# Performance work log

Measured on AMD Instinct MI355X. Metric: run time of the kernel, lower is better.

## Reference

```python
import jax, jax.numpy as jnp
import numpy as np

N = 50000      # nodes
E = 800000     # edges (avg degree 16)
D_IN = 128     # input_dim
H = 64         # hidden_dim (== output_dim)
L = 3          # num_layers


def setup_inputs() -> dict:
    key = jax.random.key(0)
    ks = jax.random.split(key, 24)
    s = 0.05
    p = lambda k, shape: jax.random.normal(k, shape, dtype=jnp.float32) * s
    inp = {}
    inp["node_features"] = jax.random.normal(ks[0], (N, D_IN), dtype=jnp.float32)
    inp["edge_index"] = jax.random.randint(ks[1], (2, E), 0, N, dtype=jnp.int32)
    # pre_mlp: Linear-ReLU-Linear (setup_LRL_nn with hidden_sizes=[hidden_dim])
    inp["pre_w1"] = p(ks[2], (D_IN, H)); inp["pre_b1"] = jnp.zeros((H,), jnp.float32)
    inp["pre_w2"] = p(ks[3], (H, H));    inp["pre_b2"] = jnp.zeros((H,), jnp.float32)
    # learnable skip gates (initialized to ones as in the module)
    inp["skip"] = jnp.ones((L, L), jnp.float32)
    # SAGEConv layers: lin_l (on mean-aggregated neighbors, with bias) + lin_r (root)
    for i in range(L):
        din = H * (i + 1)
        inp[f"wl{i}"] = p(ks[4 + 3 * i], (din, H))
        inp[f"bl{i}"] = jnp.zeros((H,), jnp.float32)
        inp[f"wr{i}"] = p(ks[5 + 3 * i], (din, H))
    # post_mlp: 256->64, 64->64, 64->256, 256->64
    inp["post_w1"] = p(ks[14], (H * (L + 1), H)); inp["post_b1"] = jnp.zeros((H,), jnp.float32)
    inp["post_w2"] = p(ks[15], (H, H));           inp["post_b2"] = jnp.zeros((H,), jnp.float32)
    inp["post_w3"] = p(ks[16], (H, 256));         inp["post_b3"] = jnp.zeros((256,), jnp.float32)
    inp["post_w4"] = p(ks[17], (256, H));         inp["post_b4"] = jnp.zeros((H,), jnp.float32)
    return inp


def _sage(x, src, dst, inv_deg, wl, bl, wr):
    # PyG SAGEConv (mean aggr): lin_l(mean_{j->i} x_j) + lin_r(x_i)
    agg = jax.ops.segment_sum(x[src], dst, num_segments=N) * inv_deg  # [N, Din]
    return agg @ wl + bl + x @ wr


def reference(node_features, edge_index,
              pre_w1, pre_b1, pre_w2, pre_b2, skip,
              wl0, bl0, wr0, wl1, bl1, wr1, wl2, bl2, wr2,
              post_w1, post_b1, post_w2, post_b2, post_w3, post_b3, post_w4, post_b4):
    src, dst = edge_index[0], edge_index[1]
    deg = jax.ops.segment_sum(jnp.ones((E,), jnp.float32), dst, num_segments=N)
    inv_deg = (1.0 / jnp.maximum(deg, 1.0))[:, None]  # [N,1]

    # pre_mlp
    x = jax.nn.relu(node_features @ pre_w1 + pre_b1) @ pre_w2 + pre_b2  # [N,H]

    layers = [(wl0, bl0, wr0), (wl1, bl1, wr1), (wl2, bl2, wr2)]
    all_emb = [x]
    emb = x
    for i, (wl, bl, wr) in enumerate(layers):
        gates = jax.nn.sigmoid(skip[i, :i + 1])  # [i+1]
        curr = jnp.concatenate([all_emb[j] * gates[j] for j in range(i + 1)], axis=1)  # [N, H*(i+1)]
        h = jax.nn.relu(_sage(curr, src, dst, inv_deg, wl, bl, wr))  # [N,H]  (dropout p=0)
        emb = jnp.concatenate([emb, h], axis=1)
        all_emb.append(h)

    s = jnp.sum(emb, axis=-2)  # sums over all nodes -> [H*(L+1)] (faithful to source)
    h = jax.nn.leaky_relu(s @ post_w1 + post_b1, negative_slope=0.1)
    h = jax.nn.relu(h @ post_w2 + post_b2)
    h = jax.nn.relu(h @ post_w3 + post_b3)
    return h @ post_w4 + post_b4  # [H]
```

## Files before the change

### kernel.cpp

```cpp
#include <hip/hip_runtime.h>
#include <math.h>

#define NN 50000
#define NE 800000
#define NB 196
#define PBH 8192

typedef float v4f __attribute__((ext_vector_type(4)));
typedef float v2f __attribute__((ext_vector_type(2)));
typedef _Float16 v8h __attribute__((ext_vector_type(8)));

__device__ __forceinline__ unsigned char enc8(float v) {
#if __has_builtin(__builtin_amdgcn_cvt_pk_fp8_f32)
  return (unsigned char)(__builtin_amdgcn_cvt_pk_fp8_f32(v, v, 0, false) & 0xFF);
#else
  unsigned u = __float_as_uint(v);
  unsigned s = (u >> 24) & 0x80u;
  unsigned au = u & 0x7fffffffu;
  float a = __uint_as_float(au);
  if (au < 0x3C800000u) {
    int m = (int)(a * 512.0f + 0.5f);
    if (m >= 8) return (unsigned char)(s | 8u);
    return (unsigned char)(s | (unsigned)m);
  }
// ... 18 lines not shown
}
#endif

__device__ __forceinline__ void dec8x8(uint2 u, float* f) {
#ifdef DEC8_HW
  v2f p0 = __builtin_amdgcn_cvt_pk_f32_fp8((int)u.x, false);
  v2f p1 = __builtin_amdgcn_cvt_pk_f32_fp8((int)u.x, true);
  v2f p2 = __builtin_amdgcn_cvt_pk_f32_fp8((int)u.y, false);
  v2f p3 = __builtin_amdgcn_cvt_pk_f32_fp8((int)u.y, true);
  f[0] = p0.x; f[1] = p0.y; f[2] = p1.x; f[3] = p1.y;
  f[4] = p2.x; f[5] = p2.y; f[6] = p3.x; f[7] = p3.y;
#else
#pragma unroll
  for (int i = 0; i < 4; ++i) f[i] = dec8_1((u.x >> (8 * i)) & 0xFF);
#pragma unroll
  for (int i = 0; i < 4; ++i) f[4 + i] = dec8_1((u.y >> (8 * i)) & 0xFF);
#endif
}
__device__ __forceinline__ void dec8x16(uint4 u, float* f) {
  dec8x8(make_uint2(u.x, u.y), f);
  dec8x8(make_uint2(u.z, u.w), f + 8);
}


__global__ __launch_bounds__(256) void k_bhist(const int* __restrict__ dst,
                                               int* __restrict__ gbcnt) {
  __shared__ int lcnt[NB];
  int t = threadIdx.x;
  for (int i = t; i < NB; i += 256) lcnt[i] = 0;
  __syncthreads();
  int eb = blockIdx.x * 4096;
#pragma unroll
  for (int i = 0; i < 16; ++i) {
    int e = eb + i * 256 + t;
    if (e < NE) atomicAdd(&lcnt[dst[e] >> 8], 1);
  }
  __syncthreads();
  for (int i = t; i < NB; i += 256)
    if (lcnt[i]) atomicAdd(&gbcnt[i], lcnt[i]);
}

__global__ __launch_bounds__(256) void k_bscan(const int* __restrict__ gbcnt,
                                               int* __restrict__ boff,
                                               int* __restrict__ gcur,
                                               int* __restrict__ offs,
                                               float* __restrict__ sv) {
// ... 102 lines not shown
#pragma unroll
  for (int i = 0; i < 4; ++i)
    *(float4*)&sw[i * 1024 + t * 4] = *(const float4*)(w + i * 1024 + t * 4);
  float gs = 1.f;
  if (A.gidx[b] >= 0) gs = 1.f / (1.f + __expf(-A.skip[A.gidx[b]]));
  __syncthreads();
#pragma unroll
  for (int i = 0; i < 4; ++i) {
    int u = t * 4 + i;
    int lane = u & 63, ct = (u >> 6) & 3, hl = (u >> 8) & 1, ks = (u >> 9) & 1;
    v8h val;
#pragma unroll
    for (int j = 0; j < 8; ++j) {
      int k = ks * 32 + ((lane >> 4) & 3) * 8 + j;
      int n = ct * 16 + (lane & 15);
      float f = sw[k * 64 + n] * gs;
      _Float16 h = (_Float16)f;
      val[j] = hl ? (_Float16)(f - (float)h) : h;
    }
    *(v8h*)(A.outp + (size_t)b * PBH + (size_t)u * 8) = val;
  }
}

struct LinArgs {
  const _Float16* a[6];
  int pb[6];
  int nsrc;
  int fusedsrc;
  const unsigned char* feat8;
  const int* offs;
  const int* csr;
  const float* invd;
  _Float16* mout;
  const _Float16* wp;
  const float* bias;
  _Float16* outp;
  unsigned char* out8;
  float* colsum;
  int n;
  int relu;
};

__global__ __launch_bounds__(512) void k_linear(LinArgs A) {
  __shared__ _Float16 atile[64 * 72];
  __shared__ float cbuf[64 * 65];
  const int t    = threadIdx.x;
  const int lane = t & 63;
  const int w    = t >> 6;
  const int wq   = w & 3;
  const int sg   = w >> 2;
  const int qd   = lane >> 4;
  const int ln   = lane & 15;
  const int n0   = blockIdx.x * 64;

  if (A.fusedsrc >= 0) {
    const int nd = t >> 3;
    const int sl = (t >> 2) & 1;
    const int q  = t & 3;
    const int node = n0 + nd;
    float a[16];
#pragma unroll
    for (int i = 0; i < 16; ++i) a[i] = 0.f;
    float dinv = 0.f;
    if (node < A.n) {
      int s = A.offs[node], e = A.offs[node + 1];
      dinv = A.invd[node];
      const unsigned char* fb = A.feat8;
      if (e > s) {
        int emax = e - 1;
        for (int p0 = s; p0 < e; p0 += 8) {
          int pa = p0 + sl, pb_ = p0 + 2 + sl, pc = p0 + 4 + sl, pd = p0 + 6 + sl;
          int ja = __builtin_nontemporal_load(A.csr + (pa < emax ? pa : emax));
          int jb = __builtin_nontemporal_load(A.csr + (pb_ < emax ? pb_ : emax));
          int jc = __builtin_nontemporal_load(A.csr + (pc < emax ? pc : emax));
          int jd = __builtin_nontemporal_load(A.csr + (pd < emax ? pd : emax));
          uint4 ua = *(const uint4*)(fb + (size_t)ja * 64 + q * 16);
          uint4 ub = *(const uint4*)(fb + (size_t)jb * 64 + q * 16);
          uint4 uc = *(const uint4*)(fb + (size_t)jc * 64 + q * 16);
          uint4 ud = *(const uint4*)(fb + (size_t)jd * 64 + q * 16);
          float f[16];
          dec8x16(ua, f);
          if (pa < e) {
#pragma unroll
            for (int i = 0; i < 16; ++i) a[i] += f[i];
          }
          dec8x16(ub, f);
          if (pb_ < e) {
#pragma unroll
            for (int i = 0; i < 16; ++i) a[i] += f[i];
          }
          dec8x16(uc, f);
          if (pc < e) {
#pragma unroll
            for (int i = 0; i < 16; ++i) a[i] += f[i];
          }
          dec8x16(ud, f);
          if (pd < e) {
#pragma unroll
            for (int i = 0; i < 16; ++i) a[i] += f[i];
          }
        }
      }
    }
#pragma unroll
    for (int i = 0; i < 16; ++i) a[i] += __shfl_xor(a[i], 4, 64);
    if (sl == 0) {
      v8h o0, o1;
#pragma unroll
      for (int i = 0; i < 8; ++i) {
        o0[i] = (_Float16)(a[i] * dinv);
        o1[i] = (_Float16)(a[8 + i] * dinv);
      }
      *(v8h*)(&atile[nd * 72 + q * 16]) = o0;
      *(v8h*)(&atile[nd * 72 + q * 16 + 8]) = o1;
      if (A.mout && node < A.n) {
        *(v8h*)(A.mout + (size_t)node * 64 + q * 16) = o0;
        *(v8h*)(A.mout + (size_t)node * 64 + q * 16 + 8) = o1;
      }
    }
  }
  __syncthreads();

  v4f acc[4];
#pragma unroll
  for (int ct = 0; ct < 4; ++ct) acc[ct] = (v4f){0.f, 0.f, 0.f, 0.f};

  const int arow = n0 + wq * 16 + ln;
  const bool arv = arow < A.n;
  const int h = (A.nsrc + 1) >> 1;
  const int sbeg = sg ? h : 0;
  const int send = sg ? A.nsrc : h;
  v8h ah[2];

  for (int s = sbeg; s < send; ++s) {
    if (s == A.fusedsrc) {
      const _Float16* ph = atile + (wq * 16 + ln) * 72;
      ah[0] = *(const v8h*)(ph + qd * 8);
      ah[1] = *(const v8h*)(ph + 32 + qd * 8);
    } else if (arv) {
      const _Float16* ph = A.a[s] + (size_t)arow * 64;
      ah[0] = *(const v8h*)(ph + qd * 8);
      ah[1] = *(const v8h*)(ph + 32 + qd * 8);
    } else {
      v8h z;
#pragma unroll
      for (int j = 0; j < 8; ++j) z[j] = (_Float16)0.f;
      ah[0] = ah[1] = z;
    }
    const _Float16* pw = A.wp + (size_t)A.pb[s] * PBH;
#pragma unroll
    for (int ks = 0; ks < 2; ++ks) {
#pragma unroll
      for (int ct = 0; ct < 4; ++ct) {
        const _Float16* pf = pw + (size_t)(ks * 512 + ct * 64 + lane) * 8;
        v8h bh = *(const v8h*)(pf);
        v8h bl = *(const v8h*)(pf + 256 * 8);
        acc[ct] = __builtin_amdgcn_mfma_f32_16x16x32_f16(ah[ks], bh, acc[ct], 0, 0, 0);
        acc[ct] = __builtin_amdgcn_mfma_f32_16x16x32_f16(ah[ks], bl, acc[ct], 0, 0, 0);
      }
    }
  }

  if (sg == 1) {
#pragma unroll
    for (int ct = 0; ct < 4; ++ct)
#pragma unroll
      for (int r = 0; r < 4; ++r) {
        int nb = wq * 16 + qd * 4 + r;
        cbuf[nb * 65 + ct * 16 + ln] = acc[ct][r];
      }
  }
  __syncthreads();

  unsigned char* f8t = (unsigned char*)atile;
  float* red = (float*)&atile[2304];

  if (sg == 0) {
    float bvals[4];
#pragma unroll
    for (int ct = 0; ct < 4; ++ct) bvals[ct] = A.bias[ct * 16 + ln];
    float cs[4] = {0.f, 0.f, 0.f, 0.f};
#pragma unroll
    for (int ct = 0; ct < 4; ++ct) {
#pragma unroll
      for (int r = 0; r < 4; ++r) {
        int nb = wq * 16 + qd * 4 + r;
        int node = n0 + nb;
        float v = acc[ct][r] + cbuf[nb * 65 + ct * 16 + ln] + bvals[ct];
        if (A.relu) v = fmaxf(v, 0.f);
        if (node < A.n) {
          if (A.outp) A.outp[(size_t)node * 64 + ct * 16 + ln] = (_Float16)v;
          if (A.out8) f8t[nb * 64 + ct * 16 + ln] = enc8(v);
          cs[ct] += v;
        }
      }
    }
    if (A.colsum) {
#pragma unroll
      for (int ct = 0; ct < 4; ++ct) {
        float v = cs[ct];
        v += __shfl_xor(v, 16, 64);
        v += __shfl_xor(v, 32, 64);
        if (qd == 0) red[wq * 64 + ct * 16 + ln] = v;
      }
    }
  }
  if (A.out8 || A.colsum) __syncthreads();
  if (A.out8 && t < 256) {
    int row = t >> 2, ch = t & 3;
    if (n0 + row < A.n) {
      uint4 val = *(const uint4*)(f8t + row * 64 + ch * 16);
      *(uint4*)(A.out8 + (size_t)(n0 + row) * 64 + ch * 16) = val;
    }
  }
  if (A.colsum && t < 64) {
    float ssum = red[t] + red[64 + t] + red[128 + t] + red[192 + t];
    atomicAdd(&A.colsum[t], ssum);
  }
}

__global__ __launch_bounds__(256) void k_pre(
    const float* __restrict__ nf, const _Float16* __restrict__ wp,
    const float* __restrict__ b1, const float* __restrict__ b2,
    _Float16* __restrict__ xout, unsigned char* __restrict__ x8,
    float* __restrict__ colsum, int n) {
  __shared__ _Float16 atile[64 * 72];
  const int t    = threadIdx.x;
  const int lane = t & 63;
  const int wv   = t >> 6;
  const int qd   = lane >> 4;
  const int ln   = lane & 15;
  const int n0   = blockIdx.x * 64;
  const int arow = n0 + wv * 16 + ln;
  const bool arv = arow < n;

  v4f acc[4];
#pragma unroll
  for (int ct = 0; ct < 4; ++ct) acc[ct] = (v4f){0.f, 0.f, 0.f, 0.f};
  v8h ah[2];

  auto domfma = [&](int pbi) {
    const _Float16* pw = wp + (size_t)pbi * PBH;
#pragma unroll
    for (int ks = 0; ks < 2; ++ks) {
#pragma unroll
      for (int ct = 0; ct < 4; ++ct) {
        const _Float16* pf = pw + (size_t)(ks * 512 + ct * 64 + lane) * 8;
        v8h bh = *(const v8h*)(pf);
        v8h bl = *(const v8h*)(pf + 256 * 8);
        acc[ct] = __builtin_amdgcn_mfma_f32_16x16x32_f16(ah[ks], bh, acc[ct], 0, 0, 0);
        acc[ct] = __builtin_amdgcn_mfma_f32_16x16x32_f16(ah[ks], bl, acc[ct], 0, 0, 0);
      }
    }
  };

  for (int s = 0; s < 2; ++s) {
#pragma unroll
    for (int ks = 0; ks < 2; ++ks) {
      v8h hv;
      if (arv) {
        const float* p = nf + (size_t)arow * 128 + s * 64 + ks * 32 + qd * 8;
        float4 u0 = *(const float4*)(p);
        float4 u1 = *(const float4*)(p + 4);
        hv[0] = (_Float16)u0.x; hv[1] = (_Float16)u0.y;
        hv[2] = (_Float16)u0.z; hv[3] = (_Float16)u0.w;
        hv[4] = (_Float16)u1.x; hv[5] = (_Float16)u1.y;
        hv[6] = (_Float16)u1.z; hv[7] = (_Float16)u1.w;
      } else {
#pragma unroll
        for (int j = 0; j < 8; ++j) hv[j] = (_Float16)0.f;
      }
      ah[ks] = hv;
    }
    domfma(s);
  }

  float b1v[4];
#pragma unroll
  for (int ct = 0; ct < 4; ++ct) b1v[ct] = b1[ct * 16 + ln];
#pragma unroll
  for (int ct = 0; ct < 4; ++ct) {
#pragma unroll
    for (int r = 0; r < 4; ++r) {
      int nb = wv * 16 + qd * 4 + r;
      float v = fmaxf(acc[ct][r] + b1v[ct], 0.f);
      atile[nb * 72 + ct * 16 + ln] = (_Float16)v;
    }
  }
#pragma unroll
  for (int ct = 0; ct < 4; ++ct) acc[ct] = (v4f){0.f, 0.f, 0.f, 0.f};
  __syncthreads();

  {
    const _Float16* ph = atile + (wv * 16 + ln) * 72;
    ah[0] = *(const v8h*)(ph + qd * 8);
    ah[1] = *(const v8h*)(ph + 32 + qd * 8);
  }
  domfma(2);

  float b2v[4];
#pragma unroll
  for (int ct = 0; ct < 4; ++ct) b2v[ct] = b2[ct * 16 + ln];

  __syncthreads();
  unsigned char* f8t = (unsigned char*)atile;
  float* red = (float*)&atile[2304];
  float cs[4] = {0.f, 0.f, 0.f, 0.f};
#pragma unroll
  for (int ct = 0; ct < 4; ++ct) {
#pragma unroll
    for (int r = 0; r < 4; ++r) {
      int nb = wv * 16 + qd * 4 + r;
      int node = n0 + nb;
      float v = acc[ct][r] + b2v[ct];
      if (node < n) {
        xout[(size_t)node * 64 + ct * 16 + ln] = (_Float16)v;
        f8t[nb * 64 + ct * 16 + ln] = enc8(v);
        cs[ct] += v;
      }
    }
  }
#pragma unroll
  for (int ct = 0; ct < 4; ++ct) {
    float v = cs[ct];
    v += __shfl_xor(v, 16, 64);
    v += __shfl_xor(v, 32, 64);
    if (qd == 0) red[wv * 64 + ct * 16 + ln] = v;
  }
  __syncthreads();
  {
    int row = t >> 2, ch = t & 3;
    if (n0 + row < n) {
      uint4 val = *(const uint4*)(f8t + row * 64 + ch * 16);
      *(uint4*)(x8 + (size_t)(n0 + row) * 64 + ch * 16) = val;
    }
  }
  if (t < 64) {
    float ssum = red[t] + red[64 + t] + red[128 + t] + red[192 + t];
    atomicAdd(&colsum[t], ssum);
  }
}

__global__ __launch_bounds__(256) void k_post(const float* __restrict__ s,
                                              const float* __restrict__ w1, const float* __restrict__ b1,
                                              const float* __restrict__ w2, const float* __restrict__ b2,
                                              const float* __restrict__ w3, const float* __restrict__ b3,
                                              const float* __restrict__ w4, const float* __restrict__ b4,
                                              float* __restrict__ outp) {
  __shared__ float sh[256], h1[64], h2[64], h3[256];
  int t = threadIdx.x;
  sh[t] = s[t];
  __syncthreads();
  if (t < 64) {
    float a = b1[t];
    for (int k = 0; k < 256; ++k) a += sh[k] * w1[k * 64 + t];
    h1[t] = (a >= 0.f) ? a : 0.1f * a;
  }
  __syncthreads();
  if (t < 64) {
    float a = b2[t];
    for (int k = 0; k < 64; ++k) a += h1[k] * w2[k * 64 + t];
    h2[t] = fmaxf(a, 0.f);
  }
  __syncthreads();
  {
    float a = b3[t];
    for (int k = 0; k < 64; ++k) a += h2[k] * w3[k * 256 + t];
    h3[t] = fmaxf(a, 0.f);
  }
  __syncthreads();
  if (t < 64) {
    float a = b4[t];
    for (int k = 0; k < 256; ++k) a += h3[k] * w4[k * 64 + t];
    outp[t] = a;
  }
}

extern "C" void kernel_launch(void* const* d_in, const int* in_sizes, int n_in,
                              void* d_out, int out_size, void* d_ws, size_t ws_size,
                              hipStream_t stream) {
  const float* nf     = (const float*)d_in[0];
  const int*   ei     = (const int*)d_in[1];
  const float* pre_w1 = (const float*)d_in[2];
  const float* pre_b1 = (const float*)d_in[3];
  const float* pre_w2 = (const float*)d_in[4];
  const float* pre_b2 = (const float*)d_in[5];
  const float* skip   = (const float*)d_in[6];
  const float* wl0 = (const float*)d_in[7],  *bl0 = (const float*)d_in[8],  *wr0 = (const float*)d_in[9];
  const float* wl1 = (const float*)d_in[10], *bl1 = (const float*)d_in[11], *wr1 = (const float*)d_in[12];
  const float* wl2 = (const float*)d_in[13], *bl2 = (const float*)d_in[14], *wr2 = (const float*)d_in[15];
  const float* pw1 = (const float*)d_in[16], *pb1 = (const float*)d_in[17];
  const float* pw2 = (const float*)d_in[18], *pb2 = (const float*)d_in[19];
  const float* pw3 = (const float*)d_in[20], *pb3 = (const float*)d_in[21];
  const float* pw4 = (const float*)d_in[22], *pb4 = (const float*)d_in[23];
  float* out = (float*)d_out;

  const int N = NN, E = NE;

  char* ws = (char*)d_ws;
  size_t pos = 0;
  auto alloc = [&](size_t bytes) {
    char* p = ws + pos;
    pos += (bytes + 255) & ~(size_t)255;
    return (void*)p;
  };
  int*      gbcnt = (int*)alloc((size_t)NB * 4);
  int*      boff  = (int*)alloc((size_t)(NB + 1) * 4);
  int*      gcur  = (int*)alloc((size_t)NB * 4);
  unsigned* ebuf  = (unsigned*)alloc((size_t)E * 4);
  int*      offs  = (int*)alloc((size_t)(N + 1) * 4);
  float*    invd  = (float*)alloc((size_t)N * 4);
  int*      csr   = (int*)alloc((size_t)E * 4);
  const size_t PB = (size_t)N * 64 * 2;
  _Float16* x  = (_Float16*)alloc(PB);
  _Float16* h0 = (_Float16*)alloc(PB);
  _Float16* h1 = (_Float16*)alloc(PB);
  _Float16* m0 = (_Float16*)alloc(PB);
  _Float16* m1 = (_Float16*)alloc(PB);
  unsigned char* f8 = (unsigned char*)alloc((size_t)N * 64);
  _Float16* wpk = (_Float16*)alloc((size_t)15 * PBH * 2);
  float* sv = (float*)alloc(256 * 4);

  hipMemsetAsync(gbcnt, 0, (size_t)NB * 4, stream);

  {
    WPackArgs W;
    const float* wsrc[15] = {pre_w1, pre_w1 + 64 * 64, pre_w2,
                             wl0, wr0,
                             wl1, wl1 + 64 * 64, wr1, wr1 + 64 * 64,
                             wl2, wl2 + 64 * 64, wl2 + 128 * 64,
                             wr2, wr2 + 64 * 64, wr2 + 128 * 64};
    const int gi[15] = {-1, -1, -1, 0, 0, 3, 4, 3, 4, 6, 7, 8, 6, 7, 8};
    for (int i = 0; i < 15; ++i) { W.w[i] = wsrc[i]; W.gidx[i] = gi[i]; }
    W.skip = skip; W.outp = wpk;
    k_wpack<<<15, 256, 0, stream>>>(W);
  }

  const int* e_src = ei;
  const int* e_dst = ei + E;
  const int EGRID = (E + 4095) / 4096;
  k_bhist<<<EGRID, 256, 0, stream>>>(e_dst, gbcnt);
  k_bscan<<<1, 256, 0, stream>>>(gbcnt, boff, gcur, offs, sv);
  k_bscatter<<<EGRID, 256, 0, stream>>>(e_src, e_dst, gcur, ebuf);
  k_bbuild<<<NB, 256, 0, stream>>>(ebuf, boff, offs, invd, csr);

  const int LGRID = (N + 63) / 64;
  auto lin = [&](int nsrc, int fusedsrc, _Float16* mout,
                 const _Float16* a0, int p0, const _Float16* a1, int p1,
                 const _Float16* a2, int p2, const _Float16* a3, int p3,
                 const _Float16* a4, int p4, const _Float16* a5, int p5,
                 const float* bias, _Float16* op, unsigned char* o8,
                 float* colsum, int relu) {
    LinArgs A;
    A.a[0] = a0; A.a[1] = a1; A.a[2] = a2; A.a[3] = a3; A.a[4] = a4; A.a[5] = a5;
    A.pb[0] = p0; A.pb[1] = p1; A.pb[2] = p2; A.pb[3] = p3; A.pb[4] = p4; A.pb[5] = p5;
    A.nsrc = nsrc; A.fusedsrc = fusedsrc;
    A.feat8 = f8; A.offs = offs; A.csr = csr; A.invd = invd;
    A.mout = mout; A.wp = wpk;
    A.bias = bias; A.outp = op; A.out8 = o8; A.colsum = colsum;
    A.n = N; A.relu = relu;
    k_linear<<<LGRID, 512, 0, stream>>>(A);
  };

  k_pre<<<LGRID, 256, 0, stream>>>(nf, wpk, pre_b1, pre_b2, x, f8, sv, N);

  lin(2, 0, m0,
      nullptr, 3, x, 4,
      nullptr, 0, nullptr, 0, nullptr, 0, nullptr, 0,
      bl0, h0, f8, sv + 64, 1);

  lin(4, 1, m1,
      m0, 5, nullptr, 6, x, 7, h0, 8,
      nullptr, 0, nullptr, 0,
      bl1, h1, f8, sv + 128, 1);

  lin(6, 2, nullptr,
      m0, 9, m1, 10, nullptr, 11, x, 12, h0, 13, h1, 14,
      bl2, nullptr, nullptr, sv + 192, 1);

  k_post<<<1, 256, 0, stream>>>(sv, pw1, pb1, pw2, pb2, pw3, pb3, pw4, pb4, out);
}
```

Before: 334.5 us.

## Fuse graph build and all layers into two cooperative grid-synced kernels

```diff
diff --git a/kernel.cpp b/kernel.cpp
--- a/kernel.cpp
+++ b/kernel.cpp
@@ -1,5 +1,8 @@
 #include <hip/hip_runtime.h>
+#include <hip/hip_cooperative_groups.h>
 #include <math.h>
+
+namespace cg = cooperative_groups;
 
 #define NN 50000
 #define NE 800000
@@ -64,6 +67,484 @@
   dec8x8(make_uint2(u.z, u.w), f + 8);
 }
 
+struct GArgs {
+  const int* esrc; const int* edst;
+  int* gbcnt; int* boff; int* gcur; int* offs; float* invd; int* csr;
+  unsigned* ebuf; float* sv;
+  const float* w[15]; int gidx[15]; const float* skip; _Float16* wpk;
+};
+
+__global__ __launch_bounds__(256) void k_graph(GArgs A) {
+  cg::grid_group grid = cg::this_grid();
+  __shared__ int s0[NB];
+  __shared__ int s1[256];
+  __shared__ int s2[256];
+  __shared__ float sw[4096];
+  const int b = blockIdx.x, t = threadIdx.x;
+
+  if (t == 0) A.gbcnt[b] = 0;
+  if (b == 0) A.sv[t] = 0.f;
+  grid.sync();
+
+  for (int i = t; i < NB; i += 256) s0[i] = 0;
+  __syncthreads();
+  const int eb = b * 4096;
+#pragma unroll
+  for (int i = 0; i < 16; ++i) {
+    int e = eb + i * 256 + t;
+    if (e < NE) atomicAdd(&s0[A.edst[e] >> 8], 1);
+  }
+  __syncthreads();
+  for (int i = t; i < NB; i += 256)
+    if (s0[i]) atomicAdd(&A.gbcnt[i], s0[i]);
+  grid.sync();
+
+  if (b == 0) {
+    int v = (t < NB) ? A.gbcnt[t] : 0;
+    s1[t] = v;
+    __syncthreads();
+    for (int o = 1; o < 256; o <<= 1) {
+      int u = (t >= o) ? s1[t - o] : 0;
+      __syncthreads();
+      s1[t] += u;
+      __syncthreads();
+    }
+    if (t < NB) { int x = s1[t] - v; A.boff[t] = x; A.gcur[t] = x; }
+    if (t == NB - 1) A.boff[NB] = s1[t];
+    if (t == 0) A.offs[NN] = NE;
+  }
+  grid.sync();
+
+  for (int i = t; i < NB; i += 256) s0[i] = 0;
+  __syncthreads();
+  unsigned pk[16]; int bk[16], lp[16];
+#pragma unroll
+  for (int i = 0; i < 16; ++i) {
+    int e = eb + i * 256 + t;
+    if (e < NE) {
+      int d = A.edst[e];
+      int bb = d >> 8;
+      pk[i] = ((unsigned)A.esrc[e] << 8) | (unsigned)(d & 255);
+      bk[i] = bb;
+      lp[i] = atomicAdd(&s0[bb], 1);
+    }
+  }
+  __syncthreads();
+  for (int i = t; i < NB; i += 256)
+    s1[i] = s0[i] ? atomicAdd(&A.gcur[i], s0[i]) : 0;
+  __syncthreads();
+#pragma unroll
+  for (int i = 0; i < 16; ++i) {
+    int e = eb + i * 256 + t;
+    if (e < NE) A.ebuf[s1[bk[i]] + lp[i]] = pk[i];
+  }
+  grid.sync();
+
+  {
+    int node0 = b << 8;
+    int es = A.boff[b], ee = A.boff[b + 1];
+    s2[t] = 0;
+    __syncthreads();
+    for (int e = es + t; e < ee; e += 256) atomicAdd(&s2[A.ebuf[e] & 255], 1);
+    __syncthreads();
+    int v = s2[t];
+    s1[t] = v;
+    __syncthreads();
+    for (int o = 1; o < 256; o <<= 1) {
+      int u = (t >= o) ? s1[t - o] : 0;
+      __syncthreads();
+      s1[t] += u;
+      __syncthreads();
+    }
+    int excl = s1[t] - v;
+    int node = node0 + t;
+    if (node < NN) {
+      A.offs[node] = es + excl;
+      A.invd[node] = 1.0f / fmaxf((float)v, 1.0f);
+    }
+    __syncthreads();
+    s1[t] = es + excl;
+    __syncthreads();
+    for (int e = es + t; e < ee; e += 256) {
+      unsigned pk2 = A.ebuf[e];
+      int p = atomicAdd(&s1[pk2 & 255], 1);
+      A.csr[p] = (int)(pk2 >> 8);
+    }
+  }
+
+  if (b < 15) {
+    const float* w = A.w[b];
+#pragma unroll
+    for (int i = 0; i < 4; ++i)
+      *(float4*)&sw[i * 1024 + t * 4] = *(const float4*)(w + i * 1024 + t * 4);
+    float gs = 1.f;
+    if (A.gidx[b] >= 0) gs = 1.f / (1.f + __expf(-A.skip[A.gidx[b]]));
+    __syncthreads();
+#pragma unroll
+    for (int i = 0; i < 4; ++i) {
+      int u = t * 4 + i;
+      int lane = u & 63, ct = (u >> 6) & 3, hl = (u >> 8) & 1, ks = (u >> 9) & 1;
+      v8h val;
+#pragma unroll
+      for (int j = 0; j < 8; ++j) {
+        int k = ks * 32 + ((lane >> 4) & 3) * 8 + j;
+        int n = ct * 16 + (lane & 15);
+        float f = sw[k * 64 + n] * gs;
+        _Float16 h = (_Float16)f;
+        val[j] = hl ? (_Float16)(f - (float)h) : h;
+      }
+      *(v8h*)(A.wpk + (size_t)b * PBH + (size_t)u * 8) = val;
+    }
+  }
+}
+
+struct CArgs {
+  const float* nf; const _Float16* wpk;
+  const float* preb1; const float* preb2;
+  const float* bl0; const float* bl1; const float* bl2;
+  const int* offs; const int* csr; const float* invd;
+  _Float16 *x, *h0, *h1, *m0, *m1;
+  unsigned char *f8a, *f8b;
+  float* sv;
+  const float *pw1, *pb1, *pw2, *pb2, *pw3, *pb3, *pw4, *pb4;
+  float* outp;
+  int n;
+};
+
+__device__ __forceinline__ void gather_tile(int t, int n0,
+    const unsigned char* __restrict__ fb, const int* __restrict__ offs,
+    const int* __restrict__ csr, const float* __restrict__ invd,
+    _Float16* atile, _Float16* mout, int n) {
+  const int nd = t >> 2, q = t & 3;
+  const int node = n0 + nd;
+  float a[16];
+#pragma unroll
+  for (int i = 0; i < 16; ++i) a[i] = 0.f;
+  float dinv = 0.f;
+  if (node < n) {
+    int s = offs[node], e = offs[node + 1];
+    dinv = invd[node];
+    int p = s;
+    for (; p + 4 <= e; p += 4) {
+      int j0 = __builtin_nontemporal_load(csr + p);
+      int j1 = __builtin_nontemporal_load(csr + p + 1);
+      int j2 = __builtin_nontemporal_load(csr + p + 2);
+      int j3 = __builtin_nontemporal_load(csr + p + 3);
+      uint4 u0 = *(const uint4*)(fb + (size_t)j0 * 64 + q * 16);
+      uint4 u1 = *(const uint4*)(fb + (size_t)j1 * 64 + q * 16);
+      uint4 u2 = *(const uint4*)(fb + (size_t)j2 * 64 + q * 16);
+      uint4 u3 = *(const uint4*)(fb + (size_t)j3 * 64 + q * 16);
+      float f0[16], f1[16], f2[16], f3[16];
+      dec8x16(u0, f0); dec8x16(u1, f1); dec8x16(u2, f2); dec8x16(u3, f3);
+#pragma unroll
+      for (int i = 0; i < 16; ++i) a[i] += (f0[i] + f1[i]) + (f2[i] + f3[i]);
+    }
+    for (; p < e; ++p) {
+      int j = __builtin_nontemporal_load(csr + p);
+      uint4 u = *(const uint4*)(fb + (size_t)j * 64 + q * 16);
+      float f[16];
+      dec8x16(u, f);
+#pragma unroll
+      for (int i = 0; i < 16; ++i) a[i] += f[i];
+    }
+  }
+  v8h o0, o1;
+#pragma unroll
+  for (int i = 0; i < 8; ++i) {
+    o0[i] = (_Float16)(a[i] * dinv);
+    o1[i] = (_Float16)(a[8 + i] * dinv);
+  }
+  *(v8h*)(&atile[nd * 72 + q * 16]) = o0;
+  *(v8h*)(&atile[nd * 72 + q * 16 + 8]) = o1;
+  if (mout && node < n) {
+    *(v8h*)(mout + (size_t)node * 64 + q * 16) = o0;
+    *(v8h*)(mout + (size_t)node * 64 + q * 16 + 8) = o1;
+  }
+}
+
+template <int NSRC, int FUSED>
+__device__ __forceinline__ void lin_tile(int t, int tile, const CArgs& A,
+    _Float16* atile,
+    const _Float16* a0, const _Float16* a1, const _Float16* a2,
+    const _Float16* a3, const _Float16* a4, const _Float16* a5,
+    int pb0, int pb1, int pb2, int pb3, int pb4, int pb5,
+    const unsigned char* gtab, const float* bias,
+    _Float16* outp, unsigned char* out8, _Float16* mout, float* colsum) {
+  const int lane = t & 63;
+  const int wv   = t >> 6;
+  const int qd   = lane >> 4;
+  const int ln   = lane & 15;
+  const int n0   = tile * 64;
+
+  gather_tile(t, n0, gtab, A.offs, A.csr, A.invd, atile, mout, A.n);
+  __syncthreads();
+
+  v4f acc[4];
+#pragma unroll
+  for (int ct = 0; ct < 4; ++ct) acc[ct] = (v4f){0.f, 0.f, 0.f, 0.f};
+
+  const int arow = n0 + wv * 16 + ln;
+  const bool arv = arow < A.n;
+  const _Float16* srcs[6] = {a0, a1, a2, a3, a4, a5};
+  const int pbs[6] = {pb0, pb1, pb2, pb3, pb4, pb5};
+
+#pragma unroll
+  for (int s = 0; s < NSRC; ++s) {
+    v8h ah0, ah1;
+    if (s == FUSED) {
+      const _Float16* ph = atile + (wv * 16 + ln) * 72;
+      ah0 = *(const v8h*)(ph + qd * 8);
+      ah1 = *(const v8h*)(ph + 32 + qd * 8);
+    } else if (arv) {
+      const _Float16* ph = srcs[s] + (size_t)arow * 64;
+      ah0 = *(const v8h*)(ph + qd * 8);
+      ah1 = *(const v8h*)(ph + 32 + qd * 8);
+    } else {
+      v8h z;
+#pragma unroll
+      for (int j = 0; j < 8; ++j) z[j] = (_Float16)0.f;
+      ah0 = ah1 = z;
+    }
+    const _Float16* pw = A.wpk + (size_t)pbs[s] * PBH;
+#pragma unroll
+    for (int ct = 0; ct < 4; ++ct) {
+      const _Float16* pf0 = pw + (size_t)(ct * 64 + lane) * 8;
+      const _Float16* pf1 = pw + (size_t)(512 + ct * 64 + lane) * 8;
+      v8h bh0 = *(const v8h*)(pf0);
+      v8h bl0v = *(const v8h*)(pf0 + 2048);
+      v8h bh1 = *(const v8h*)(pf1);
+      v8h bl1v = *(const v8h*)(pf1 + 2048);
+      acc[ct] = __builtin_amdgcn_mfma_f32_16x16x32_f16(ah0, bh0, acc[ct], 0, 0, 0);
+      acc[ct] = __builtin_amdgcn_mfma_f32_16x16x32_f16(ah0, bl0v, acc[ct], 0, 0, 0);
+      acc[ct] = __builtin_amdgcn_mfma_f32_16x16x32_f16(ah1, bh1, acc[ct], 0, 0, 0);
+      acc[ct] = __builtin_amdgcn_mfma_f32_16x16x32_f16(ah1, bl1v, acc[ct], 0, 0, 0);
+    }
+  }
+
+  float bvals[4];
+#pragma unroll
+  for (int ct = 0; ct < 4; ++ct) bvals[ct] = bias[ct * 16 + ln];
+
+  __syncthreads();
+  unsigned char* f8t = (unsigned char*)atile;
+  float* red = (float*)&atile[2304];
+
+  float cs[4] = {0.f, 0.f, 0.f, 0.f};
+#pragma unroll
+  for (int ct = 0; ct < 4; ++ct) {
+#pragma unroll
+    for (int r = 0; r < 4; ++r) {
+      int nb = wv * 16 + qd * 4 + r;
+      int node = n0 + nb;
+      float v = fmaxf(acc[ct][r] + bvals[ct], 0.f);
+      if (node < A.n) {
+        if (outp) outp[(size_t)node * 64 + ct * 16 + ln] = (_Float16)v;
+        if (out8) f8t[nb * 64 + ct * 16 + ln] = enc8(v);
+        cs[ct] += v;
+      }
+    }
+  }
+#pragma unroll
+  for (int ct = 0; ct < 4; ++ct) {
+    float v = cs[ct];
+    v += __shfl_xor(v, 16, 64);
+    v += __shfl_xor(v, 32, 64);
+    if (qd == 0) red[wv * 64 + ct * 16 + ln] = v;
+  }
+  __syncthreads();
+  if (out8) {
+    int row = t >> 2, ch = t & 3;
+    if (n0 + row < A.n) {
+      uint4 val = *(const uint4*)(f8t + row * 64 + ch * 16);
+      *(uint4*)(out8 + (size_t)(n0 + row) * 64 + ch * 16) = val;
+    }
+  }
+  if (t < 64) {
+    float ssum = red[t] + red[64 + t] + red[128 + t] + red[192 + t];
+    atomicAdd(&colsum[t], ssum);
+  }
+}
+
+__device__ __forceinline__ void pre_tile(int t, int tile, const CArgs& A,
+                                         _Float16* atile) {
+  const int lane = t & 63;
+  const int wv   = t >> 6;
+  const int qd   = lane >> 4;
+  const int ln   = lane & 15;
+  const int n0   = tile * 64;
+  const int arow = n0 + wv * 16 + ln;
+  const bool arv = arow < A.n;
+
+  v4f acc[4];
+#pragma unroll
+  for (int ct = 0; ct < 4; ++ct) acc[ct] = (v4f){0.f, 0.f, 0.f, 0.f};
+  v8h ah[2];
+
+  auto domfma = [&](int pbi) {
+    const _Float16* pw = A.wpk + (size_t)pbi * PBH;
+#pragma unroll
+    for (int ks = 0; ks < 2; ++ks) {
+#pragma unroll
+      for (int ct = 0; ct < 4; ++ct) {
+        const _Float16* pf = pw + (size_t)(ks * 512 + ct * 64 + lane) * 8;
+        v8h bh = *(const v8h*)(pf);
+        v8h bl = *(const v8h*)(pf + 2048);
+        acc[ct] = __builtin_amdgcn_mfma_f32_16x16x32_f16(ah[ks], bh, acc[ct], 0, 0, 0);
+        acc[ct] = __builtin_amdgcn_mfma_f32_16x16x32_f16(ah[ks], bl, acc[ct], 0, 0, 0);
+      }
+    }
+  };
+
+  for (int s = 0; s < 2; ++s) {
+#pragma unroll
+    for (int ks = 0; ks < 2; ++ks) {
+      v8h hv;
+      if (arv) {
+        const float* p = A.nf + (size_t)arow * 128 + s * 64 + ks * 32 + qd * 8;
+        float4 u0 = *(const float4*)(p);
+        float4 u1 = *(const float4*)(p + 4);
+        hv[0] = (_Float16)u0.x; hv[1] = (_Float16)u0.y;
+        hv[2] = (_Float16)u0.z; hv[3] = (_Float16)u0.w;
+        hv[4] = (_Float16)u1.x; hv[5] = (_Float16)u1.y;
+        hv[6] = (_Float16)u1.z; hv[7] = (_Float16)u1.w;
+      } else {
+#pragma unroll
+        for (int j = 0; j < 8; ++j) hv[j] = (_Float16)0.f;
+      }
+      ah[ks] = hv;
+    }
+    domfma(s);
+  }
+
+  float b1v[4];
+#pragma unroll
+  for (int ct = 0; ct < 4; ++ct) b1v[ct] = A.preb1[ct * 16 + ln];
+#pragma unroll
+  for (int ct = 0; ct < 4; ++ct) {
+#pragma unroll
+    for (int r = 0; r < 4; ++r) {
+      int nb = wv * 16 + qd * 4 + r;
+      float v = fmaxf(acc[ct][r] + b1v[ct], 0.f);
+      atile[nb * 72 + ct * 16 + ln] = (_Float16)v;
+    }
+  }
+#pragma unroll
+  for (int ct = 0; ct < 4; ++ct) acc[ct] = (v4f){0.f, 0.f, 0.f, 0.f};
+  __syncthreads();
+
+  {
+    const _Float16* ph = atile + (wv * 16 + ln) * 72;
+    ah[0] = *(const v8h*)(ph + qd * 8);
+    ah[1] = *(const v8h*)(ph + 32 + qd * 8);
+  }
+  domfma(2);
+
+  float b2v[4];
+#pragma unroll
+  for (int ct = 0; ct < 4; ++ct) b2v[ct] = A.preb2[ct * 16 + ln];
+
+  __syncthreads();
+  unsigned char* f8t = (unsigned char*)atile;
+  float* red = (float*)&atile[2304];
+  float cs[4] = {0.f, 0.f, 0.f, 0.f};
+#pragma unroll
+  for (int ct = 0; ct < 4; ++ct) {
+#pragma unroll
+    for (int r = 0; r < 4; ++r) {
+      int nb = wv * 16 + qd * 4 + r;
+      int node = n0 + nb;
+      float v = acc[ct][r] + b2v[ct];
+      if (node < A.n) {
+        A.x[(size_t)node * 64 + ct * 16 + ln] = (_Float16)v;
+        f8t[nb * 64 + ct * 16 + ln] = enc8(v);
+        cs[ct] += v;
+      }
+    }
+  }
+#pragma unroll
+  for (int ct = 0; ct < 4; ++ct) {
+    float v = cs[ct];
+    v += __shfl_xor(v, 16, 64);
+    v += __shfl_xor(v, 32, 64);
+    if (qd == 0) red[wv * 64 + ct * 16 + ln] = v;
+  }
+  __syncthreads();
+  {
+    int row = t >> 2, ch = t & 3;
+    if (n0 + row < A.n) {
+      uint4 val = *(const uint4*)(f8t + row * 64 + ch * 16);
+      *(uint4*)(A.f8a + (size_t)(n0 + row) * 64 + ch * 16) = val;
+    }
+  }
+  if (t < 64) {
+    float ssum = red[t] + red[64 + t] + red[128 + t] + red[192 + t];
+    atomicAdd(&A.sv[t], ssum);
+  }
+}
+
+__device__ __forceinline__ void post_body(int tt, const CArgs& A, float* Lf) {
+  float* sh = Lf; float* h1 = Lf + 256; float* h2 = Lf + 320; float* h3 = Lf + 384;
+  if (tt < 256) sh[tt] = A.sv[tt];
+  __syncthreads();
+  if (tt < 64) {
+    float a = A.pb1[tt];
+    for (int k = 0; k < 256; ++k) a += sh[k] * A.pw1[k * 64 + tt];
+    h1[tt] = (a >= 0.f) ? a : 0.1f * a;
+  }
+  __syncthreads();
+  if (tt < 64) {
+    float a = A.pb2[tt];
+    for (int k = 0; k < 64; ++k) a += h1[k] * A.pw2[k * 64 + tt];
+    h2[tt] = fmaxf(a, 0.f);
+  }
+  __syncthreads();
+  if (tt < 256) {
+    float a = A.pb3[tt];
+    for (int k = 0; k < 64; ++k) a += h2[k] * A.pw3[k * 256 + tt];
+    h3[tt] = fmaxf(a, 0.f);
+  }
+  __syncthreads();
+  if (tt < 64) {
+    float a = A.pb4[tt];
+    for (int k = 0; k < 256; ++k) a += h3[k] * A.pw4[k * 64 + tt];
+    A.outp[tt] = a;
+  }
+}
+
+__global__ __launch_bounds__(512, 4) void k_compute(CArgs A) {
+  cg::grid_group grid = cg::this_grid();
+  __shared__ _Float16 atile[2][64 * 72];
+  const int t    = threadIdx.x & 255;
+  const int hb   = threadIdx.x >> 8;
+  const int tile = blockIdx.x * 2 + hb;
+
+  pre_tile(t, tile, A, atile[hb]);
+  __threadfence();
+  grid.sync();
+
+  lin_tile<2, 0>(t, tile, A, atile[hb],
+                 nullptr, A.x, nullptr, nullptr, nullptr, nullptr,
+                 3, 4, 0, 0, 0, 0,
+                 A.f8a, A.bl0, A.h0, A.f8b, A.m0, A.sv + 64);
+  __threadfence();
+  grid.sync();
+
+  lin_tile<4, 1>(t, tile, A, atile[hb],
+                 A.m0, nullptr, A.x, A.h0, nullptr, nullptr,
+                 5, 6, 7, 8, 0, 0,
+                 A.f8b, A.bl1, A.h1, A.f8a, A.m1, A.sv + 128);
+  __threadfence();
+  grid.sync();
+
+  lin_tile<6, 2>(t, tile, A, atile[hb],
+                 A.m0, A.m1, nullptr, A.x, A.h0, A.h1,
+                 9, 10, 11, 12, 13, 14,
+                 A.f8a, A.bl2, nullptr, nullptr, nullptr, A.sv + 192);
+  __threadfence();
+  grid.sync();
+
+  if (blockIdx.x == 0) post_body(threadIdx.x, A, (float*)&atile[0][0]);
+}
 
 __global__ __launch_bounds__(256) void k_bhist(const int* __restrict__ dst,
                                                int* __restrict__ gbcnt) {
@@ -212,358 +693,36 @@
   }
 }
 
-struct LinArgs {
+struct FLinArgs {
+  CArgs C;
   const _Float16* a[6];
   int pb[6];
   int nsrc;
-  int fusedsrc;
-  const unsigned char* feat8;
-  const int* offs;
-  const int* csr;
-  const float* invd;
-  _Float16* mout;
-  const _Float16* wp;
+  const unsigned char* gtab;
   const float* bias;
   _Float16* outp;
   unsigned char* out8;
+  _Float16* mout;
   float* colsum;
-  int n;
-  int relu;
 };
 
-__global__ __launch_bounds__(512) void k_linear(LinArgs A) {
+template <int NSRC, int FUSED>
+__global__ __launch_bounds__(256) void k_linF(FLinArgs F) {
   __shared__ _Float16 atile[64 * 72];
-  __shared__ float cbuf[64 * 65];
-  const int t    = threadIdx.x;
-  const int lane = t & 63;
-  const int w    = t >> 6;
-  const int wq   = w & 3;
-  const int sg   = w >> 2;
-  const int qd   = lane >> 4;
-  const int ln   = lane & 15;
-  const int n0   = blockIdx.x * 64;
-
-  if (A.fusedsrc >= 0) {
-    const int nd = t >> 3;
-    const int sl = (t >> 2) & 1;
-    const int q  = t & 3;
-    const int node = n0 + nd;
-    float a[16];
-#pragma unroll
-    for (int i = 0; i < 16; ++i) a[i] = 0.f;
-    float dinv = 0.f;
-    if (node < A.n) {
-      int s = A.offs[node], e = A.offs[node + 1];
-      dinv = A.invd[node];
-      const unsigned char* fb = A.feat8;
-      if (e > s) {
-        int emax = e - 1;
-        for (int p0 = s; p0 < e; p0 += 8) {
-          int pa = p0 + sl, pb_ = p0 + 2 + sl, pc = p0 + 4 + sl, pd = p0 + 6 + sl;
-          int ja = __builtin_nontemporal_load(A.csr + (pa < emax ? pa : emax));
-          int jb = __builtin_nontemporal_load(A.csr + (pb_ < emax ? pb_ : emax));
-          int jc = __builtin_nontemporal_load(A.csr + (pc < emax ? pc : emax));
-          int jd = __builtin_nontemporal_load(A.csr + (pd < emax ? pd : emax));
-          uint4 ua = *(const uint4*)(fb + (size_t)ja * 64 + q * 16);
-          uint4 ub = *(const uint4*)(fb + (size_t)jb * 64 + q * 16);
-          uint4 uc = *(const uint4*)(fb + (size_t)jc * 64 + q * 16);
-          uint4 ud = *(const uint4*)(fb + (size_t)jd * 64 + q * 16);
-          float f[16];
-          dec8x16(ua, f);
-          if (pa < e) {
-#pragma unroll
-            for (int i = 0; i < 16; ++i) a[i] += f[i];
-          }
-          dec8x16(ub, f);
-          if (pb_ < e) {
-#pragma unroll
-            for (int i = 0; i < 16; ++i) a[i] += f[i];
-          }
-          dec8x16(uc, f);
-          if (pc < e) {
-#pragma unroll
-            for (int i = 0; i < 16; ++i) a[i] += f[i];
-          }
-          dec8x16(ud, f);
-          if (pd < e) {
-#pragma unroll
-            for (int i = 0; i < 16; ++i) a[i] += f[i];
-          }
-        }
-      }
-    }
-#pragma unroll
-    for (int i = 0; i < 16; ++i) a[i] += __shfl_xor(a[i], 4, 64);
-    if (sl == 0) {
-      v8h o0, o1;
-#pragma unroll
-      for (int i = 0; i < 8; ++i) {
-        o0[i] = (_Float16)(a[i] * dinv);
-        o1[i] = (_Float16)(a[8 + i] * dinv);
-      }
-      *(v8h*)(&atile[nd * 72 + q * 16]) = o0;
-      *(v8h*)(&atile[nd * 72 + q * 16 + 8]) = o1;
-      if (A.mout && node < A.n) {
-        *(v8h*)(A.mout + (size_t)node * 64 + q * 16) = o0;
-        *(v8h*)(A.mout + (size_t)node * 64 + q * 16 + 8) = o1;
-      }
-    }
-  }
-  __syncthreads();
-
-  v4f acc[4];
-#pragma unroll
-  for (int ct = 0; ct < 4; ++ct) acc[ct] = (v4f){0.f, 0.f, 0.f, 0.f};
-
-  const int arow = n0 + wq * 16 + ln;
-  const bool arv = arow < A.n;
-  const int h = (A.nsrc + 1) >> 1;
-  const int sbeg = sg ? h : 0;
-  const int send = sg ? A.nsrc : h;
-  v8h ah[2];
-
-  for (int s = sbeg; s < send; ++s) {
-    if (s == A.fusedsrc) {
-      const _Float16* ph = atile + (wq * 16 + ln) * 72;
-      ah[0] = *(const v8h*)(ph + qd * 8);
-      ah[1] = *(const v8h*)(ph + 32 + qd * 8);
-    } else if (arv) {
-      const _Float16* ph = A.a[s] + (size_t)arow * 64;
-      ah[0] = *(const v8h*)(ph + qd * 8);
-      ah[1] = *(const v8h*)(ph + 32 + qd * 8);
-    } else {
-      v8h z;
-#pragma unroll
-      for (int j = 0; j < 8; ++j) z[j] = (_Float16)0.f;
-      ah[0] = ah[1] = z;
-    }
-    const _Float16* pw = A.wp + (size_t)A.pb[s] * PBH;
-#pragma unroll
-    for (int ks = 0; ks < 2; ++ks) {
-#pragma unroll
-      for (int ct = 0; ct < 4; ++ct) {
-        const _Float16* pf = pw + (size_t)(ks * 512 + ct * 64 + lane) * 8;
-        v8h bh = *(const v8h*)(pf);
-        v8h bl = *(const v8h*)(pf + 256 * 8);
-        acc[ct] = __builtin_amdgcn_mfma_f32_16x16x32_f16(ah[ks], bh, acc[ct], 0, 0, 0);
-        acc[ct] = __builtin_amdgcn_mfma_f32_16x16x32_f16(ah[ks], bl, acc[ct], 0, 0, 0);
-      }
-    }
-  }
-
-  if (sg == 1) {
-#pragma unroll
-    for (int ct = 0; ct < 4; ++ct)
-#pragma unroll
-      for (int r = 0; r < 4; ++r) {
-        int nb = wq * 16 + qd * 4 + r;
-        cbuf[nb * 65 + ct * 16 + ln] = acc[ct][r];
-      }
-  }
-  __syncthreads();
-
-  unsigned char* f8t = (unsigned char*)atile;
-  float* red = (float*)&atile[2304];
-
-  if (sg == 0) {
-    float bvals[4];
-#pragma unroll
-    for (int ct = 0; ct < 4; ++ct) bvals[ct] = A.bias[ct * 16 + ln];
-    float cs[4] = {0.f, 0.f, 0.f, 0.f};
-#pragma unroll
-    for (int ct = 0; ct < 4; ++ct) {
-#pragma unroll
-      for (int r = 0; r < 4; ++r) {
-        int nb = wq * 16 + qd * 4 + r;
-        int node = n0 + nb;
-        float v = acc[ct][r] + cbuf[nb * 65 + ct * 16 + ln] + bvals[ct];
-        if (A.relu) v = fmaxf(v, 0.f);
-        if (node < A.n) {
-          if (A.outp) A.outp[(size_t)node * 64 + ct * 16 + ln] = (_Float16)v;
-          if (A.out8) f8t[nb * 64 + ct * 16 + ln] = enc8(v);
-          cs[ct] += v;
-        }
-      }
-    }
-    if (A.colsum) {
-#pragma unroll
-      for (int ct = 0; ct < 4; ++ct) {
-        float v = cs[ct];
-        v += __shfl_xor(v, 16, 64);
-        v += __shfl_xor(v, 32, 64);
-        if (qd == 0) red[wq * 64 + ct * 16 + ln] = v;
-      }
-    }
-  }
-  if (A.out8 || A.colsum) __syncthreads();
-  if (A.out8 && t < 256) {
-    int row = t >> 2, ch = t & 3;
-    if (n0 + row < A.n) {
-      uint4 val = *(const uint4*)(f8t + row * 64 + ch * 16);
-      *(uint4*)(A.out8 + (size_t)(n0 + row) * 64 + ch * 16) = val;
-    }
-  }
-  if (A.colsum && t < 64) {
-    float ssum = red[t] + red[64 + t] + red[128 + t] + red[192 + t];
-    atomicAdd(&A.colsum[t], ssum);
-  }
-}
-
-__global__ __launch_bounds__(256) void k_pre(
-    const float* __restrict__ nf, const _Float16* __restrict__ wp,
-    const float* __restrict__ b1, const float* __restrict__ b2,
-    _Float16* __restrict__ xout, unsigned char* __restrict__ x8,
-    float* __restrict__ colsum, int n) {
+  lin_tile<NSRC, FUSED>(threadIdx.x, blockIdx.x, F.C, atile,
+                        F.a[0], F.a[1], F.a[2], F.a[3], F.a[4], F.a[5],
+                        F.pb[0], F.pb[1], F.pb[2], F.pb[3], F.pb[4], F.pb[5],
+                        F.gtab, F.bias, F.outp, F.out8, F.mout, F.colsum);
+}
+
+__global__ __launch_bounds__(256) void k_preF(CArgs A) {
   __shared__ _Float16 atile[64 * 72];
-  const int t    = threadIdx.x;
-  const int lane = t & 63;
-  const int wv   = t >> 6;
-  const int qd   = lane >> 4;
-  const int ln   = lane & 15;
-  const int n0   = blockIdx.x * 64;
-  const int arow = n0 + wv * 16 + ln;
-  const bool arv = arow < n;
-
-  v4f acc[4];
-#pragma unroll
-  for (int ct = 0; ct < 4; ++ct) acc[ct] = (v4f){0.f, 0.f, 0.f, 0.f};
-  v8h ah[2];
-
-  auto domfma = [&](int pbi) {
-    const _Float16* pw = wp + (size_t)pbi * PBH;
-#pragma unroll
-    for (int ks = 0; ks < 2; ++ks) {
-#pragma unroll
-      for (int ct = 0; ct < 4; ++ct) {
-        const _Float16* pf = pw + (size_t)(ks * 512 + ct * 64 + lane) * 8;
-        v8h bh = *(const v8h*)(pf);
-        v8h bl = *(const v8h*)(pf + 256 * 8);
-        acc[ct] = __builtin_amdgcn_mfma_f32_16x16x32_f16(ah[ks], bh, acc[ct], 0, 0, 0);
-        acc[ct] = __builtin_amdgcn_mfma_f32_16x16x32_f16(ah[ks], bl, acc[ct], 0, 0, 0);
-      }
-    }
-  };
-
-  for (int s = 0; s < 2; ++s) {
-#pragma unroll
-    for (int ks = 0; ks < 2; ++ks) {
-      v8h hv;
-      if (arv) {
-        const float* p = nf + (size_t)arow * 128 + s * 64 + ks * 32 + qd * 8;
-        float4 u0 = *(const float4*)(p);
-        float4 u1 = *(const float4*)(p + 4);
-        hv[0] = (_Float16)u0.x; hv[1] = (_Float16)u0.y;
-        hv[2] = (_Float16)u0.z; hv[3] = (_Float16)u0.w;
-        hv[4] = (_Float16)u1.x; hv[5] = (_Float16)u1.y;
-        hv[6] = (_Float16)u1.z; hv[7] = (_Float16)u1.w;
-      } else {
-#pragma unroll
-        for (int j = 0; j < 8; ++j) hv[j] = (_Float16)0.f;
-      }
-      ah[ks] = hv;
-    }
-    domfma(s);
-  }
-
-  float b1v[4];
-#pragma unroll
-  for (int ct = 0; ct < 4; ++ct) b1v[ct] = b1[ct * 16 + ln];
-#pragma unroll
-  for (int ct = 0; ct < 4; ++ct) {
-#pragma unroll
-    for (int r = 0; r < 4; ++r) {
-      int nb = wv * 16 + qd * 4 + r;
-      float v = fmaxf(acc[ct][r] + b1v[ct], 0.f);
-      atile[nb * 72 + ct * 16 + ln] = (_Float16)v;
-    }
-  }
-#pragma unroll
-  for (int ct = 0; ct < 4; ++ct) acc[ct] = (v4f){0.f, 0.f, 0.f, 0.f};
-  __syncthreads();
-
-  {
-    const _Float16* ph = atile + (wv * 16 + ln) * 72;
-    ah[0] = *(const v8h*)(ph + qd * 8);
-    ah[1] = *(const v8h*)(ph + 32 + qd * 8);
-  }
-  domfma(2);
-
-  float b2v[4];
-#pragma unroll
-  for (int ct = 0; ct < 4; ++ct) b2v[ct] = b2[ct * 16 + ln];
-
-  __syncthreads();
-  unsigned char* f8t = (unsigned char*)atile;
-  float* red = (float*)&atile[2304];
-  float cs[4] = {0.f, 0.f, 0.f, 0.f};
-#pragma unroll
-  for (int ct = 0; ct < 4; ++ct) {
-#pragma unroll
-    for (int r = 0; r < 4; ++r) {
-      int nb = wv * 16 + qd * 4 + r;
-      int node = n0 + nb;
-      float v = acc[ct][r] + b2v[ct];
-      if (node < n) {
-        xout[(size_t)node * 64 + ct * 16 + ln] = (_Float16)v;
-        f8t[nb * 64 + ct * 16 + ln] = enc8(v);
-        cs[ct] += v;
-      }
-    }
-  }
-#pragma unroll
-  for (int ct = 0; ct < 4; ++ct) {
-    float v = cs[ct];
-    v += __shfl_xor(v, 16, 64);
-    v += __shfl_xor(v, 32, 64);
-    if (qd == 0) red[wv * 64 + ct * 16 + ln] = v;
-  }
-  __syncthreads();
-  {
-    int row = t >> 2, ch = t & 3;
-    if (n0 + row < n) {
-      uint4 val = *(const uint4*)(f8t + row * 64 + ch * 16);
-      *(uint4*)(x8 + (size_t)(n0 + row) * 64 + ch * 16) = val;
-    }
-  }
-  if (t < 64) {
-    float ssum = red[t] + red[64 + t] + red[128 + t] + red[192 + t];
-    atomicAdd(&colsum[t], ssum);
-  }
-}
-
-__global__ __launch_bounds__(256) void k_post(const float* __restrict__ s,
-                                              const float* __restrict__ w1, const float* __restrict__ b1,
-                                              const float* __restrict__ w2, const float* __restrict__ b2,
-                                              const float* __restrict__ w3, const float* __restrict__ b3,
-                                              const float* __restrict__ w4, const float* __restrict__ b4,
-                                              float* __restrict__ outp) {
-  __shared__ float sh[256], h1[64], h2[64], h3[256];
-  int t = threadIdx.x;
-  sh[t] = s[t];
-  __syncthreads();
-  if (t < 64) {
-    float a = b1[t];
-    for (int k = 0; k < 256; ++k) a += sh[k] * w1[k * 64 + t];
-    h1[t] = (a >= 0.f) ? a : 0.1f * a;
-  }
-  __syncthreads();
-  if (t < 64) {
-    float a = b2[t];
-    for (int k = 0; k < 64; ++k) a += h1[k] * w2[k * 64 + t];
-    h2[t] = fmaxf(a, 0.f);
-  }
-  __syncthreads();
-  {
-    float a = b3[t];
-    for (int k = 0; k < 64; ++k) a += h2[k] * w3[k * 256 + t];
-    h3[t] = fmaxf(a, 0.f);
-  }
-  __syncthreads();
-  if (t < 64) {
-    float a = b4[t];
-    for (int k = 0; k < 256; ++k) a += h3[k] * w4[k * 64 + t];
-    outp[t] = a;
-  }
+  pre_tile(threadIdx.x, blockIdx.x, A, atile);
+}
+
+__global__ __launch_bounds__(256) void k_postF(CArgs A) {
+  __shared__ float Lf[640];
+  post_body(threadIdx.x, A, Lf);
 }
 
 extern "C" void kernel_launch(void* const* d_in, const int* in_sizes, int n_in,
@@ -607,66 +766,84 @@
   _Float16* h1 = (_Float16*)alloc(PB);
   _Float16* m0 = (_Float16*)alloc(PB);
   _Float16* m1 = (_Float16*)alloc(PB);
-  unsigned char* f8 = (unsigned char*)alloc((size_t)N * 64);
+  unsigned char* f8a = (unsigned char*)alloc((size_t)N * 64);
+  unsigned char* f8b = (unsigned char*)alloc((size_t)N * 64);
   _Float16* wpk = (_Float16*)alloc((size_t)15 * PBH * 2);
   float* sv = (float*)alloc(256 * 4);
 
-  hipMemsetAsync(gbcnt, 0, (size_t)NB * 4, stream);
-
-  {
+  const int* e_src = ei;
+  const int* e_dst = ei + E;
+  const float* wsrc[15] = {pre_w1, pre_w1 + 64 * 64, pre_w2,
+                           wl0, wr0,
+                           wl1, wl1 + 64 * 64, wr1, wr1 + 64 * 64,
+                           wl2, wl2 + 64 * 64, wl2 + 128 * 64,
+                           wr2, wr2 + 64 * 64, wr2 + 128 * 64};
+  const int gi[15] = {-1, -1, -1, 0, 0, 3, 4, 3, 4, 6, 7, 8, 6, 7, 8};
+
+  GArgs G;
+  G.esrc = e_src; G.edst = e_dst;
+  G.gbcnt = gbcnt; G.boff = boff; G.gcur = gcur; G.offs = offs;
+  G.invd = invd; G.csr = csr; G.ebuf = ebuf; G.sv = sv;
+  for (int i = 0; i < 15; ++i) { G.w[i] = wsrc[i]; G.gidx[i] = gi[i]; }
+  G.skip = skip; G.wpk = wpk;
+  void* gp[] = {(void*)&G};
+  hipError_t eg = hipLaunchCooperativeKernel((void*)k_graph, dim3(NB), dim3(256),
+                                             gp, 0, stream);
+  if (eg != hipSuccess) {
+    hipMemsetAsync(gbcnt, 0, (size_t)NB * 4, stream);
     WPackArgs W;
-    const float* wsrc[15] = {pre_w1, pre_w1 + 64 * 64, pre_w2,
-                             wl0, wr0,
-                             wl1, wl1 + 64 * 64, wr1, wr1 + 64 * 64,
-                             wl2, wl2 + 64 * 64, wl2 + 128 * 64,
-                             wr2, wr2 + 64 * 64, wr2 + 128 * 64};
-    const int gi[15] = {-1, -1, -1, 0, 0, 3, 4, 3, 4, 6, 7, 8, 6, 7, 8};
     for (int i = 0; i < 15; ++i) { W.w[i] = wsrc[i]; W.gidx[i] = gi[i]; }
     W.skip = skip; W.outp = wpk;
     k_wpack<<<15, 256, 0, stream>>>(W);
-  }
-
-  const int* e_src = ei;
-  const int* e_dst = ei + E;
-  const int EGRID = (E + 4095) / 4096;
-  k_bhist<<<EGRID, 256, 0, stream>>>(e_dst, gbcnt);
-  k_bscan<<<1, 256, 0, stream>>>(gbcnt, boff, gcur, offs, sv);
-  k_bscatter<<<EGRID, 256, 0, stream>>>(e_src, e_dst, gcur, ebuf);
-  k_bbuild<<<NB, 256, 0, stream>>>(ebuf, boff, offs, invd, csr);
-
-  const int LGRID = (N + 63) / 64;
-  auto lin = [&](int nsrc, int fusedsrc, _Float16* mout,
-                 const _Float16* a0, int p0, const _Float16* a1, int p1,
-                 const _Float16* a2, int p2, const _Float16* a3, int p3,
-                 const _Float16* a4, int p4, const _Float16* a5, int p5,
-                 const float* bias, _Float16* op, unsigned char* o8,
-                 float* colsum, int relu) {
-    LinArgs A;
-    A.a[0] = a0; A.a[1] = a1; A.a[2] = a2; A.a[3] = a3; A.a[4] = a4; A.a[5] = a5;
-    A.pb[0] = p0; A.pb[1] = p1; A.pb[2] = p2; A.pb[3] = p3; A.pb[4] = p4; A.pb[5] = p5;
-    A.nsrc = nsrc; A.fusedsrc = fusedsrc;
-    A.feat8 = f8; A.offs = offs; A.csr = csr; A.invd = invd;
-    A.mout = mout; A.wp = wpk;
-    A.bias = bias; A.outp = op; A.out8 = o8; A.colsum = colsum;
-    A.n = N; A.relu = relu;
-    k_linear<<<LGRID, 512, 0, stream>>>(A);
-  };
-
-  k_pre<<<LGRID, 256, 0, stream>>>(nf, wpk, pre_b1, pre_b2, x, f8, sv, N);
-
-  lin(2, 0, m0,
-      nullptr, 3, x, 4,
-      nullptr, 0, nullptr, 0, nullptr, 0, nullptr, 0,
-      bl0, h0, f8, sv + 64, 1);
-
-  lin(4, 1, m1,
-      m0, 5, nullptr, 6, x, 7, h0, 8,
-      nullptr, 0, nullptr, 0,
-      bl1, h1, f8, sv + 128, 1);
-
-  lin(6, 2, nullptr,
-      m0, 9, m1, 10, nullptr, 11, x, 12, h0, 13, h1, 14,
-      bl2, nullptr, nullptr, sv + 192, 1);
-
-  k_post<<<1, 256, 0, stream>>>(sv, pw1, pb1, pw2, pb2, pw3, pb3, pw4, pb4, out);
-}
+    const int EGRID = (E + 4095) / 4096;
+    k_bhist<<<EGRID, 256, 0, stream>>>(e_dst, gbcnt);
+    k_bscan<<<1, 256, 0, stream>>>(gbcnt, boff, gcur, offs, sv);
+    k_bscatter<<<EGRID, 256, 0, stream>>>(e_src, e_dst, gcur, ebuf);
+    k_bbuild<<<NB, 256, 0, stream>>>(ebuf, boff, offs, invd, csr);
+  }
+
+  CArgs C;
+  C.nf = nf; C.wpk = wpk; C.preb1 = pre_b1; C.preb2 = pre_b2;
+  C.bl0 = bl0; C.bl1 = bl1; C.bl2 = bl2;
+  C.offs = offs; C.csr = csr; C.invd = invd;
+  C.x = x; C.h0 = h0; C.h1 = h1; C.m0 = m0; C.m1 = m1;
+  C.f8a = f8a; C.f8b = f8b; C.sv = sv;
+  C.pw1 = pw1; C.pb1 = pb1; C.pw2 = pw2; C.pb2 = pb2;
+  C.pw3 = pw3; C.pb3 = pb3; C.pw4 = pw4; C.pb4 = pb4;
+  C.outp = out; C.n = N;
+  void* cp[] = {(void*)&C};
+  hipError_t ec = hipLaunchCooperativeKernel((void*)k_compute, dim3(391), dim3(512),
+                                             cp, 0, stream);
+  if (ec != hipSuccess) {
+    const int LGRID = (N + 63) / 64;
+    k_preF<<<LGRID, 256, 0, stream>>>(C);
+    {
+      FLinArgs F; F.C = C;
+      F.a[0] = nullptr; F.a[1] = x; F.a[2] = nullptr; F.a[3] = nullptr;
+      F.a[4] = nullptr; F.a[5] = nullptr;
+      F.pb[0] = 3; F.pb[1] = 4; F.pb[2] = 0; F.pb[3] = 0; F.pb[4] = 0; F.pb[5] = 0;
+      F.nsrc = 2; F.gtab = f8a; F.bias = bl0;
+      F.outp = h0; F.out8 = f8b; F.mout = m0; F.colsum = sv + 64;
+      k_linF<2, 0><<<LGRID, 256, 0, stream>>>(F);
+    }
+    {
+      FLinArgs F; F.C = C;
+      F.a[0] = m0; F.a[1] = nullptr; F.a[2] = x; F.a[3] = h0;
+      F.a[4] = nullptr; F.a[5] = nullptr;
+      F.pb[0] = 5; F.pb[1] = 6; F.pb[2] = 7; F.pb[3] = 8; F.pb[4] = 0; F.pb[5] = 0;
+      F.nsrc = 4; F.gtab = f8b; F.bias = bl1;
+      F.outp = h1; F.out8 = f8a; F.mout = m1; F.colsum = sv + 128;
+      k_linF<4, 1><<<LGRID, 256, 0, stream>>>(F);
+    }
+    {
+      FLinArgs F; F.C = C;
+      F.a[0] = m0; F.a[1] = m1; F.a[2] = nullptr; F.a[3] = x;
+      F.a[4] = h0; F.a[5] = h1;
+      F.pb[0] = 9; F.pb[1] = 10; F.pb[2] = 11; F.pb[3] = 12; F.pb[4] = 13; F.pb[5] = 14;
+      F.nsrc = 6; F.gtab = f8a; F.bias = bl2;
+      F.outp = nullptr; F.out8 = nullptr; F.mout = nullptr; F.colsum = sv + 192;
+      k_linF<6, 2><<<LGRID, 256, 0, stream>>>(F);
+    }
+    k_postF<<<1, 256, 0, stream>>>(C);
+  }
+}
```

After: 845.9 us. 2.53x slower.
